# Kernel optimization log

Measured on AMD Instinct MI355X. Metric: run time of the kernel, lower is better.

Reference implementation:

```python
import jax, jax.numpy as jnp
import numpy as np

WIDTH = 1024
HEAD = 64


def setup_inputs() -> dict:
    key = jax.random.key(0)
    ks = jax.random.split(key, 8)
    B, S = 8, 2048
    x = jax.random.normal(ks[0], (B, S, WIDTH), dtype=jnp.float32)
    attn_mask = jnp.ones((B, S), dtype=jnp.int32)
    s = WIDTH ** -0.5
    Wq = jax.random.normal(ks[1], (WIDTH, HEAD), dtype=jnp.float32) * s
    bq = jnp.zeros((HEAD,), dtype=jnp.float32)
    Wk = jax.random.normal(ks[2], (WIDTH, HEAD), dtype=jnp.float32) * s
    bk = jnp.zeros((HEAD,), dtype=jnp.float32)
    Wv = jax.random.normal(ks[3], (WIDTH, HEAD), dtype=jnp.float32) * s
    bv = jnp.zeros((HEAD,), dtype=jnp.float32)
    return {"x": x, "attn_mask": attn_mask, "Wq": Wq, "bq": bq,
            "Wk": Wk, "bk": bk, "Wv": Wv, "bv": bv}


def reference(x, attn_mask, Wq, bq, Wk, bk, Wv, bv):
    # x: [B, S, width]; attn_mask: [B, S] (key padding mask)
    scale = HEAD ** -0.5
    Q = x @ Wq + bq  # [B, S, H]
    K = x @ Wk + bk
    V = x @ Wv + bv
    scores = jnp.einsum('bqh,bkh->bqk', Q, K) * scale  # [B, S, S]
    mask = (attn_mask[:, None, :] != 0)  # [B, 1, S] broadcast over queries
    scores = jnp.where(mask, scores, -jnp.inf)
    A = jax.nn.softmax(scores, axis=-1)
    return jnp.einsum('bqk,bkh->bqh', A, V)
```

## Files before the change

### kernel.cpp

```cpp
#include <hip/hip_runtime.h>
#include <hip/hip_bf16.h>

#define BATCH 8
#define SEQ   2048
#define DMODEL 1024
#define HD    64

typedef __attribute__((ext_vector_type(8))) short bf16x8;
typedef __attribute__((ext_vector_type(4))) float f32x4;
typedef __attribute__((ext_vector_type(4))) int int4v;
typedef __attribute__((ext_vector_type(2))) unsigned uint2v;
typedef unsigned int u32;

__device__ inline unsigned short f2bf(float f) {
    unsigned u = __builtin_bit_cast(unsigned, f);
    unsigned r = (u + 0x7FFFu + ((u >> 16) & 1u)) >> 16;
    return (unsigned short)r;
}

__device__ inline unsigned cvtpk(float lo, float hi) {
    unsigned r;
    asm("v_cvt_pk_bf16_f32 %0, %1, %2" : "=v"(r) : "v"(lo), "v"(hi));
    return r;
}

__device__ inline void gl_lds16(const void* g, void* l) {
    __builtin_amdgcn_global_load_lds(
        (const __attribute__((address_space(1))) u32*)g,
        (__attribute__((address_space(3))) u32*)l, 16, 0, 0);
}

__global__ void prep_w(const float* __restrict__ Wq, const float* __restrict__ Wk,
                       const float* __restrict__ Wv, unsigned short* __restrict__ WFrag) {
    __shared__ float tt[64][65];
    int p = blockIdx.x >> 4;
    int t = blockIdx.x & 15;
    int k0 = t * 64;
    const float* W = (p == 0) ? Wq : (p == 1) ? Wk : Wv;
    int tid = threadIdx.x;
#pragma unroll
    for (int j = 0; j < 16; j++) {
        int idx = tid + j * 256;
        int r = idx >> 6, c = idx & 63;
        tt[r][c] = W[(size_t)(k0 + r) * HD + c];
    }
    __syncthreads();
#pragma unroll
    for (int gi = 0; gi < 2; gi++) {
        int g = tid * 2 + gi;
        int ln = g & 15, lg = (g >> 4) & 3, s = (g >> 6) & 1, n = (g >> 7) & 3;
        union { bf16x8 v; unsigned short u[8]; } pk;
#pragma unroll
        for (int e = 0; e < 8; e++)
            pk.u[e] = f2bf(tt[s * 32 + lg * 8 + e][n * 16 + ln]);
        *(bf16x8*)(WFrag + (((size_t)(p * 4 + n) * 16 + t) * 1024 + s * 512 + lg * 128 + ln * 8)) = pk.v;
    }
}

__global__ __launch_bounds__(256) void proj_kernel(
    const float* __restrict__ x,
    const float* __restrict__ bq, const float* __restrict__ bk, const float* __restrict__ bv,
    const unsigned short* __restrict__ WFrag,
    unsigned short* __restrict__ Q, unsigned short* __restrict__ K,
    unsigned short* __restrict__ VT) {

    __shared__ __align__(16) unsigned short Xls[2][32 * 64];

    int tid = threadIdx.x;
    int w = tid >> 6, lane = tid & 63;
    int lg = lane >> 4, ln = lane & 15;
    int m0 = blockIdx.x * 32;

    const unsigned short* wbase[3];
#pragma unroll
    for (int j = 0; j < 3; j++)
        wbase[j] = WFrag + (size_t)(w * 3 + j) * 16384 + lane * 8;

    f32x4 acc[2][3];
#pragma unroll
    for (int m = 0; m < 2; m++)
#pragma unroll
        for (int j = 0; j < 3; j++) acc[m][j] = (f32x4){0.f, 0.f, 0.f, 0.f};

    f32x4 xq[2][2];
    bf16x8 bset[2][6];

    auto loadX = [&](int set, int k0) {
#pragma unroll
        for (int i = 0; i < 2; i++) {
            int c = tid + i * 256;
            xq[set][i] = *(const f32x4*)(x + (size_t)(m0 + (c >> 4)) * DMODEL + k0 + (c & 15) * 4);
        }
    };
    auto writeX = [&](unsigned short* buf, int set) {
#pragma unroll
        for (int i = 0; i < 2; i++) {
            int c = tid + i * 256;
            int row = c >> 4, slot = (c & 15) >> 1, half = c & 1;
            uint2v pk;
            pk[0] = cvtpk(xq[set][i][0], xq[set][i][1]);
            pk[1] = cvtpk(xq[set][i][2], xq[set][i][3]);
            *(uint2v*)((char*)buf + row * 128 + ((slot ^ (row & 7)) << 4) + half * 8) = pk;
        }
    };
    auto loadB = [&](int set, int k0) {
        int tb = (k0 >> 6) * 1024;
#pragma unroll
        for (int s = 0; s < 2; s++)
#pragma unroll
            for (int j = 0; j < 3; j++)
                bset[set][s * 3 + j] = *(const bf16x8*)(wbase[j] + tb + s * 512);
    };

    loadX(0, 0);
    writeX(&Xls[0][0], 0);
    loadX(1, 64);
    loadX(0, 128);
    loadB(0, 0);
    loadB(1, 64);
    __syncthreads();

#pragma unroll
    for (int t = 0; t < 16; t++) {
        const int cur = t & 1;
        const char* xb = (const char*)&Xls[cur][0];

#pragma unroll
        for (int s = 0; s < 2; s++) {
            bf16x8 a[2];
#pragma unroll
            for (int m = 0; m < 2; m++) {
                int row = m * 16 + ln;
                a[m] = *(const bf16x8*)(xb + row * 128 + (((s * 4 + lg) ^ (row & 7)) << 4));
            }
            __builtin_amdgcn_s_setprio(1);
#pragma unroll
            for (int m = 0; m < 2; m++)
#pragma unroll
                for (int j = 0; j < 3; j++)
                    acc[m][j] = __builtin_amdgcn_mfma_f32_16x16x32_bf16(a[m], bset[cur][s * 3 + j], acc[m][j], 0, 0, 0);
            __builtin_amdgcn_s_setprio(0);
        }

        if (t + 2 < 16) loadB(cur, (t + 2) * 64);
        if (t < 15) {
            writeX(&Xls[cur ^ 1][0], (t + 1) & 1);
            if (t + 3 < 16) loadX((t + 1) & 1, (t + 3) * 64);
        }
        __syncthreads();
    }

#pragma unroll
    for (int j = 0; j < 3; j++) {
        int f = w * 3 + j;
        int p = f >> 2, n = f & 3;
        int col = n * 16 + ln;
        const float* bias = (p == 0) ? bq : (p == 1) ? bk : bv;
        float bb = bias[col];
#pragma unroll
        for (int m = 0; m < 2; m++) {
#pragma unroll
            for (int r = 0; r < 4; r++) {
                float v = acc[m][j][r] + bb;
                int grow = m0 + m * 16 + lg * 4 + r;
                if (p == 0)      Q[(size_t)grow * HD + col] = f2bf(v);
                else if (p == 1) K[(size_t)grow * HD + col] = f2bf(v);
                else {
                    int b2 = grow >> 11, srow = grow & (SEQ - 1);
                    VT[((size_t)b2 * HD + col) * SEQ + srow] = f2bf(v);
                }
            }
        }
    }
}

__device__ inline void stage_tile(int tid, const unsigned short* Kb, const unsigned short* VTb,
                                  int kt, unsigned short* kbuf, unsigned short* vbuf) {
#pragma unroll
    for (int i = 0; i < 2; i++) {
        int d = tid * 16 + i * 4096;
        int row = d >> 7, slot = (d >> 4) & 7;
        const unsigned short* src = Kb + (size_t)(kt + row) * HD + ((slot ^ (row & 7)) << 3);
        gl_lds16(src, (char*)kbuf + d);
    }
#pragma unroll
    for (int i = 0; i < 2; i++) {
        int d = tid * 16 + i * 4096;
        int row = d >> 7, slot = (d >> 4) & 7;
        const unsigned short* src = VTb + (size_t)row * SEQ + kt + ((slot ^ (row & 7)) << 3);
        gl_lds16(src, (char*)vbuf + d);
    }
}

__global__ __launch_bounds__(256, 4) void attn_kernel(
    const unsigned short* __restrict__ Q, const unsigned short* __restrict__ K,
    const unsigned short* __restrict__ VT, const int* __restrict__ mask,
    float* __restrict__ out,
    unsigned short* __restrict__ Op, float* __restrict__ Mp, float* __restrict__ Lp,
    int nsplit) {

    __shared__ __align__(16) unsigned short Kls[2][64 * 64];
    __shared__ __align__(16) unsigned short Vls[2][64 * 64];
    __shared__ __align__(16) unsigned short plds_[4][16 * 64];

    int tid = threadIdx.x;
    int w = tid >> 6, lane = tid & 63;
    int lg = lane >> 4, ln = lane & 15;
    int b = blockIdx.y;
    int kh = blockIdx.z;
    int q0 = blockIdx.x * 64 + w * 16;
    int ntiles = 32 / nsplit;
    int kt0 = kh * ntiles * 64;

    const float SC = 0.125f * 1.44269504088896f;

    const int* mb = mask + b * SEQ;

    bf16x8 qf[2];
    {
        const unsigned short* qptr = Q + ((size_t)b * SEQ + q0 + ln) * HD + lg * 8;
        qf[0] = *(const bf16x8*)(qptr);
        qf[1] = *(const bf16x8*)(qptr + 32);
    }

    f32x4 o[4];
#pragma unroll
    for (int n = 0; n < 4; n++) o[n] = (f32x4){0.f, 0.f, 0.f, 0.f};
    float mrun = -1e38f, lrun = 0.f;

    const unsigned short* Kb = K + (size_t)b * SEQ * HD;
    const unsigned short* VTb = VT + (size_t)b * HD * SEQ;

    unsigned short* kcur = &Kls[0][0]; unsigned short* knx = &Kls[1][0];
    unsigned short* vcur = &Vls[0][0]; unsigned short* vnx = &Vls[1][0];
    char* pl = (char*)&plds_[w][0];
    const int swz = (ln & 7) << 4;

    stage_tile(tid, Kb, VTb, kt0, kcur, vcur);
    __syncthreads();

#pragma unroll 2
    for (int tt = 0; tt < ntiles; ++tt) {
        int kt = kt0 + tt * 64;
        if (tt < ntiles - 1) stage_tile(tid, Kb, VTb, kt + 64, knx, vnx);

        int4v mi[4];
#pragma unroll
        for (int n = 0; n < 4; ++n)
            mi[n] = *(const int4v*)(mb + kt + n * 16 + lg * 4);

        f32x4 st[4];
        const char* kb = (const char*)kcur;
        __builtin_amdgcn_s_setprio(1);
#pragma unroll
        for (int n = 0; n < 4; ++n) {
            int rb = (n * 16 + ln) * 128;
            bf16x8 ka0 = *(const bf16x8*)(kb + ((rb + lg * 16) ^ swz));
            bf16x8 ka1 = *(const bf16x8*)(kb + ((rb + 64 + lg * 16) ^ swz));
            f32x4 z = (f32x4){0.f, 0.f, 0.f, 0.f};
            st[n] = __builtin_amdgcn_mfma_f32_16x16x32_bf16(ka0, qf[0], z, 0, 0, 0);
            st[n] = __builtin_amdgcn_mfma_f32_16x16x32_bf16(ka1, qf[1], st[n], 0, 0, 0);
        }
        __builtin_amdgcn_s_setprio(0);

#pragma unroll
        for (int n = 0; n < 4; ++n)
#pragma unroll
            for (int r = 0; r < 4; ++r)
                st[n][r] = fmaf(st[n][r], SC, mi[n][r] ? 0.f : -1e30f);

        f32x4 mx = st[0];
#pragma unroll
        for (int n = 1; n < 4; ++n)
#pragma unroll
            for (int r = 0; r < 4; ++r) mx[r] = fmaxf(mx[r], st[n][r]);
        float pmax = fmaxf(fmaxf(mx[0], mx[1]), fmaxf(mx[2], mx[3]));
        pmax = fmaxf(pmax, __shfl_xor(pmax, 16));
        pmax = fmaxf(pmax, __shfl_xor(pmax, 32));

        if (!__all(pmax <= mrun + 8.f)) {
            float mnew = fmaxf(mrun, pmax);
            float corr = exp2f(mrun - mnew);
            mrun = mnew;
            lrun *= corr;
            float c0 = __shfl(corr, lg * 4 + 0);
            float c1 = __shfl(corr, lg * 4 + 1);
            float c2 = __shfl(corr, lg * 4 + 2);
            float c3 = __shfl(corr, lg * 4 + 3);
#pragma unroll
            for (int n = 0; n < 4; ++n) {
                o[n][0] *= c0; o[n][1] *= c1; o[n][2] *= c2; o[n][3] *= c3;
            }
        }

        f32x4 sv = (f32x4){0.f, 0.f, 0.f, 0.f};
#pragma unroll
        for (int n = 0; n < 4; ++n)
#pragma unroll
            for (int r = 0; r < 4; ++r) {
                float pp = exp2f(st[n][r] - mrun);
                st[n][r] = pp;
                sv[r] += pp;
            }
        float ts = (sv[0] + sv[1]) + (sv[2] + sv[3]);
        ts += __shfl_xor(ts, 16);
        ts += __shfl_xor(ts, 32);
        lrun += ts;

#pragma unroll
        for (int n = 0; n < 4; ++n) {
            uint2v ww;
            ww[0] = cvtpk(st[n][0], st[n][1]);
            ww[1] = cvtpk(st[n][2], st[n][3]);
            *(uint2v*)(pl + ((ln * 128 + n * 32 + lg * 8) ^ swz)) = ww;
        }
        asm volatile("s_waitcnt lgkmcnt(0)" ::: "memory");
        __builtin_amdgcn_sched_barrier(0);
        bf16x8 pa0 = *(const bf16x8*)(pl + ((ln * 128 + lg * 16) ^ swz));
        bf16x8 pa1 = *(const bf16x8*)(pl + ((ln * 128 + 64 + lg * 16) ^ swz));

        const char* vb = (const char*)vcur;
        __builtin_amdgcn_s_setprio(1);
#pragma unroll
        for (int n = 0; n < 4; ++n) {
            int rb = (n * 16 + ln) * 128;
            bf16x8 v0 = *(const bf16x8*)(vb + ((rb + lg * 16) ^ swz));
            bf16x8 v1 = *(const bf16x8*)(vb + ((rb + 64 + lg * 16) ^ swz));
            o[n] = __builtin_amdgcn_mfma_f32_16x16x32_bf16(pa0, v0, o[n], 0, 0, 0);
            o[n] = __builtin_amdgcn_mfma_f32_16x16x32_bf16(pa1, v1, o[n], 0, 0, 0);
        }
        __builtin_amdgcn_s_setprio(0);

        __syncthreads();
        unsigned short* tk = kcur; kcur = knx; knx = tk;
        unsigned short* tv = vcur; vcur = vnx; vnx = tv;
    }

    if (nsplit == 1) {
#pragma unroll
        for (int r = 0; r < 4; r++) {
            float Lr = __shfl(lrun, lg * 4 + r);
            float inv = 1.0f / Lr;
            int row = q0 + lg * 4 + r;
#pragma unroll
            for (int n = 0; n < 4; n++)
                out[((size_t)b * SEQ + row) * HD + n * 16 + ln] = o[n][r] * inv;
        }
    } else {
        size_t base = (size_t)kh * BATCH * SEQ * HD;
#pragma unroll
        for (int r = 0; r < 4; r++) {
            int row = q0 + lg * 4 + r;
            size_t gr = (size_t)b * SEQ + row;
#pragma unroll
            for (int n = 0; n < 4; n++)
                Op[base + gr * HD + n * 16 + ln] = f2bf(o[n][r]);
        }
        if (lane < 16) {
            size_t gr = (size_t)b * SEQ + q0 + ln;
            Mp[(size_t)kh * BATCH * SEQ + gr] = mrun;
            Lp[(size_t)kh * BATCH * SEQ + gr] = lrun;
        }
    }
}

__global__ __launch_bounds__(256) void combine_kernel(
    const unsigned short* __restrict__ Op, const float* __restrict__ Mp,
    const float* __restrict__ Lp, float* __restrict__ out) {
    int g = blockIdx.x * 256 + threadIdx.x;
    int row = g >> 3;
    int c0 = (g & 7) * 8;
    const int NR = BATCH * SEQ;

    float m[4], l[4];
#pragma unroll
    for (int s = 0; s < 4; s++) {
        m[s] = Mp[(size_t)s * NR + row];
        l[s] = Lp[(size_t)s * NR + row];
    }
    float M = fmaxf(fmaxf(m[0], m[1]), fmaxf(m[2], m[3]));
    float e[4], L = 0.f;
#pragma unroll
    for (int s = 0; s < 4; s++) { e[s] = exp2f(m[s] - M); L += l[s] * e[s]; }
    float inv = 1.0f / L;

    float acc[8] = {0.f, 0.f, 0.f, 0.f, 0.f, 0.f, 0.f, 0.f};
#pragma unroll
    for (int s = 0; s < 4; s++) {
        bf16x8 ov = *(const bf16x8*)(Op + ((size_t)s * NR + row) * HD + c0);
#pragma unroll
        for (int i = 0; i < 8; i++) {
            float f = __builtin_bit_cast(float, ((u32)(unsigned short)ov[i]) << 16);
            acc[i] += f * e[s];
        }
    }
    f32x4 r0, r1;
#pragma unroll
    for (int i = 0; i < 4; i++) { r0[i] = acc[i] * inv; r1[i] = acc[4 + i] * inv; }
    *(f32x4*)(out + (size_t)row * HD + c0) = r0;
    *(f32x4*)(out + (size_t)row * HD + c0 + 4) = r1;
}

extern "C" void kernel_launch(void* const* d_in, const int* in_sizes, int n_in,
                              void* d_out, int out_size, void* d_ws, size_t ws_size,
                              hipStream_t stream) {
    const float* x  = (const float*)d_in[0];
    const int*   am = (const int*)d_in[1];
    const float* Wq = (const float*)d_in[2];
    const float* bq = (const float*)d_in[3];
    const float* Wk = (const float*)d_in[4];
    const float* bk = (const float*)d_in[5];
    const float* Wv = (const float*)d_in[6];
    const float* bv = (const float*)d_in[7];
    float* out = (float*)d_out;

    unsigned short* ws = (unsigned short*)d_ws;
    unsigned short* Wt  = ws;
    unsigned short* Qw  = ws + 3 * HD * DMODEL;
    unsigned short* Kw  = Qw + (size_t)BATCH * SEQ * HD;
    unsigned short* VTw = Kw + (size_t)BATCH * SEQ * HD;
    size_t base_sh = 3 * HD * DMODEL + 3 * (size_t)BATCH * SEQ * HD;
    unsigned short* Op = ws + base_sh;
    float* Mp = (float*)(Op + 4 * (size_t)BATCH * SEQ * HD);
    float* Lp = Mp + 4 * (size_t)BATCH * SEQ;
    size_t need = base_sh * 2 + 4 * (size_t)BATCH * SEQ * HD * 2
                + 8 * (size_t)BATCH * SEQ * 4;

    int nsplit = (ws_size >= need) ? 4 : 1;

    prep_w<<<48, 256, 0, stream>>>(Wq, Wk, Wv, Wt);
    proj_kernel<<<(BATCH * SEQ) / 32, 256, 0, stream>>>(x, bq, bk, bv, Wt, Qw, Kw, VTw);
    attn_kernel<<<dim3(SEQ / 64, BATCH, nsplit), 256, 0, stream>>>(Qw, Kw, VTw, am, out,
                                                                   Op, Mp, Lp, nsplit);
    if (nsplit == 4)
        combine_kernel<<<(BATCH * SEQ * 8) / 256, 256, 0, stream>>>(Op, Mp, Lp, out);
}
```

Measured before the change: 55.63 us.

## Load x directly into MFMA A-fragments in projection kernel, drop LDS staging

The projection kernel no longer stages x through shared memory with barriers. Each lane now reads its fp32 A-fragment rows straight from global memory, converts them to bf16 in registers and feeds the MFMAs, using a two-set register ping-pong for prefetch. Launch bounds are set to 2 blocks per CU. This removes the LDS writes and reads and the per-step __syncthreads, but each lane's global loads are less coalesced (16 rows per wave, 32 bytes per lane per chunk) and more registers are held live.

```diff
diff --git a/kernel.cpp b/kernel.cpp
--- a/kernel.cpp
+++ b/kernel.cpp
@@ -57,15 +57,13 @@
     }
 }
 
-__global__ __launch_bounds__(256) void proj_kernel(
+__global__ __launch_bounds__(256, 2) void proj_kernel(
     const float* __restrict__ x,
     const float* __restrict__ bq, const float* __restrict__ bk, const float* __restrict__ bv,
     const unsigned short* __restrict__ WFrag,
     unsigned short* __restrict__ Q, unsigned short* __restrict__ K,
     unsigned short* __restrict__ VT) {
 
-    __shared__ __align__(16) unsigned short Xls[2][32 * 64];
-
     int tid = threadIdx.x;
     int w = tid >> 6, lane = tid & 63;
     int lg = lane >> 4, ln = lane & 15;
@@ -76,78 +74,64 @@
     for (int j = 0; j < 3; j++)
         wbase[j] = WFrag + (size_t)(w * 3 + j) * 16384 + lane * 8;
 
+    const float* xr0 = x + (size_t)(m0 + ln) * DMODEL + lg * 8;
+    const float* xr1 = x + (size_t)(m0 + 16 + ln) * DMODEL + lg * 8;
+
     f32x4 acc[2][3];
 #pragma unroll
     for (int m = 0; m < 2; m++)
 #pragma unroll
         for (int j = 0; j < 3; j++) acc[m][j] = (f32x4){0.f, 0.f, 0.f, 0.f};
 
-    f32x4 xq[2][2];
-    bf16x8 bset[2][6];
-
-    auto loadX = [&](int set, int k0) {
-#pragma unroll
-        for (int i = 0; i < 2; i++) {
-            int c = tid + i * 256;
-            xq[set][i] = *(const f32x4*)(x + (size_t)(m0 + (c >> 4)) * DMODEL + k0 + (c & 15) * 4);
-        }
+    bf16x8 bA[6], bB[6];
+    f32x4 xA[8], xB[8];
+
+    auto LB = [&](bf16x8* d, int t) {
+#pragma unroll
+        for (int s = 0; s < 2; s++)
+#pragma unroll
+            for (int j = 0; j < 3; j++)
+                d[s * 3 + j] = *(const bf16x8*)(wbase[j] + t * 1024 + s * 512);
     };
-    auto writeX = [&](unsigned short* buf, int set) {
-#pragma unroll
-        for (int i = 0; i < 2; i++) {
-            int c = tid + i * 256;
-            int row = c >> 4, slot = (c & 15) >> 1, half = c & 1;
-            uint2v pk;
-            pk[0] = cvtpk(xq[set][i][0], xq[set][i][1]);
-            pk[1] = cvtpk(xq[set][i][2], xq[set][i][3]);
-            *(uint2v*)((char*)buf + row * 128 + ((slot ^ (row & 7)) << 4) + half * 8) = pk;
-        }
+    auto LX = [&](f32x4* d, int t) {
+        int k0 = t * 64;
+        d[0] = *(const f32x4*)(xr0 + k0);      d[1] = *(const f32x4*)(xr0 + k0 + 4);
+        d[2] = *(const f32x4*)(xr1 + k0);      d[3] = *(const f32x4*)(xr1 + k0 + 4);
+        d[4] = *(const f32x4*)(xr0 + k0 + 32); d[5] = *(const f32x4*)(xr0 + k0 + 36);
+        d[6] = *(const f32x4*)(xr1 + k0 + 32); d[7] = *(const f32x4*)(xr1 + k0 + 36);
     };
-    auto loadB = [&](int set, int k0) {
-        int tb = (k0 >> 6) * 1024;
-#pragma unroll
-        for (int s = 0; s < 2; s++)
-#pragma unroll
-            for (int j = 0; j < 3; j++)
-                bset[set][s * 3 + j] = *(const bf16x8*)(wbase[j] + tb + s * 512);
+    auto CP = [&](const f32x4* xd, const bf16x8* bd) {
+#pragma unroll
+        for (int s = 0; s < 2; s++) {
+            union { bf16x8 v; unsigned u[4]; } a0, a1;
+            a0.u[0] = cvtpk(xd[s * 4 + 0][0], xd[s * 4 + 0][1]);
+            a0.u[1] = cvtpk(xd[s * 4 + 0][2], xd[s * 4 + 0][3]);
+            a0.u[2] = cvtpk(xd[s * 4 + 1][0], xd[s * 4 + 1][1]);
+            a0.u[3] = cvtpk(xd[s * 4 + 1][2], xd[s * 4 + 1][3]);
+            a1.u[0] = cvtpk(xd[s * 4 + 2][0], xd[s * 4 + 2][1]);
+            a1.u[1] = cvtpk(xd[s * 4 + 2][2], xd[s * 4 + 2][3]);
+            a1.u[2] = cvtpk(xd[s * 4 + 3][0], xd[s * 4 + 3][1]);
+            a1.u[3] = cvtpk(xd[s * 4 + 3][2], xd[s * 4 + 3][3]);
+#pragma unroll
+            for (int j = 0; j < 3; j++) {
+                acc[0][j] = __builtin_amdgcn_mfma_f32_16x16x32_bf16(a0.v, bd[s * 3 + j], acc[0][j], 0, 0, 0);
+                acc[1][j] = __builtin_amdgcn_mfma_f32_16x16x32_bf16(a1.v, bd[s * 3 + j], acc[1][j], 0, 0, 0);
+            }
+        }
     };
 
-    loadX(0, 0);
-    writeX(&Xls[0][0], 0);
-    loadX(1, 64);
-    loadX(0, 128);
-    loadB(0, 0);
-    loadB(1, 64);
-    __syncthreads();
-
-#pragma unroll
-    for (int t = 0; t < 16; t++) {
-        const int cur = t & 1;
-        const char* xb = (const char*)&Xls[cur][0];
-
-#pragma unroll
-        for (int s = 0; s < 2; s++) {
-            bf16x8 a[2];
-#pragma unroll
-            for (int m = 0; m < 2; m++) {
-                int row = m * 16 + ln;
-                a[m] = *(const bf16x8*)(xb + row * 128 + (((s * 4 + lg) ^ (row & 7)) << 4));
-            }
-            __builtin_amdgcn_s_setprio(1);
-#pragma unroll
-            for (int m = 0; m < 2; m++)
-#pragma unroll
-                for (int j = 0; j < 3; j++)
-                    acc[m][j] = __builtin_amdgcn_mfma_f32_16x16x32_bf16(a[m], bset[cur][s * 3 + j], acc[m][j], 0, 0, 0);
-            __builtin_amdgcn_s_setprio(0);
-        }
-
-        if (t + 2 < 16) loadB(cur, (t + 2) * 64);
-        if (t < 15) {
-            writeX(&Xls[cur ^ 1][0], (t + 1) & 1);
-            if (t + 3 < 16) loadX((t + 1) & 1, (t + 3) * 64);
-        }
-        __syncthreads();
+    LX(xA, 0);
+    LB(bA, 0);
+#pragma unroll 1
+    for (int t = 0; t < 16; t += 2) {
+        LX(xB, t + 1);
+        LB(bB, t + 1);
+        CP(xA, bA);
+        if (t + 2 < 16) {
+            LX(xA, t + 2);
+            LB(bA, t + 2);
+        }
+        CP(xB, bB);
     }
 
 #pragma unroll
```

Result: slower. 76.70 us (+37.9%).

## Restructure projection K-loop into 128-wide tiles with ping-pong register sets

Applied to the files above, without the earlier changes.

The projection kernel now stages 128-column x tiles in LDS, using a 16-way XOR swizzle instead of 64-column tiles. It replaces the fully unrolled 16-step loop with a rolled 4-iteration loop that alternates two explicit register sets for x and B fragments. It also adds a launch_bounds minimum of 2 blocks per SM and drops the s_setprio hints. The goal is fewer barriers per K element and more overlap of global loads with MFMA work, at the cost of more registers per thread, which the occupancy hint may force to spill.

```diff
diff --git a/kernel.cpp b/kernel.cpp
--- a/kernel.cpp
+++ b/kernel.cpp
@@ -57,14 +57,14 @@
     }
 }
 
-__global__ __launch_bounds__(256) void proj_kernel(
+__global__ __launch_bounds__(256, 2) void proj_kernel(
     const float* __restrict__ x,
     const float* __restrict__ bq, const float* __restrict__ bk, const float* __restrict__ bv,
     const unsigned short* __restrict__ WFrag,
     unsigned short* __restrict__ Q, unsigned short* __restrict__ K,
     unsigned short* __restrict__ VT) {
 
-    __shared__ __align__(16) unsigned short Xls[2][32 * 64];
+    __shared__ __align__(16) unsigned short Xls[2][32 * 128];
 
     int tid = threadIdx.x;
     int w = tid >> 6, lane = tid & 63;
@@ -82,71 +82,71 @@
 #pragma unroll
         for (int j = 0; j < 3; j++) acc[m][j] = (f32x4){0.f, 0.f, 0.f, 0.f};
 
-    f32x4 xq[2][2];
-    bf16x8 bset[2][6];
-
-    auto loadX = [&](int set, int k0) {
-#pragma unroll
-        for (int i = 0; i < 2; i++) {
+    f32x4 xA[4], xB[4];
+    bf16x8 bA[12], bB[12];
+
+    auto loadX = [&](f32x4* xr, int tile) {
+#pragma unroll
+        for (int i = 0; i < 4; i++) {
             int c = tid + i * 256;
-            xq[set][i] = *(const f32x4*)(x + (size_t)(m0 + (c >> 4)) * DMODEL + k0 + (c & 15) * 4);
+            xr[i] = *(const f32x4*)(x + (size_t)(m0 + (c >> 5)) * DMODEL + tile * 128 + (c & 31) * 4);
         }
     };
-    auto writeX = [&](unsigned short* buf, int set) {
-#pragma unroll
-        for (int i = 0; i < 2; i++) {
+    auto writeX = [&](unsigned short* buf, const f32x4* xr) {
+#pragma unroll
+        for (int i = 0; i < 4; i++) {
             int c = tid + i * 256;
-            int row = c >> 4, slot = (c & 15) >> 1, half = c & 1;
+            int row = c >> 5, cc = c & 31;
             uint2v pk;
-            pk[0] = cvtpk(xq[set][i][0], xq[set][i][1]);
-            pk[1] = cvtpk(xq[set][i][2], xq[set][i][3]);
-            *(uint2v*)((char*)buf + row * 128 + ((slot ^ (row & 7)) << 4) + half * 8) = pk;
+            pk[0] = cvtpk(xr[i][0], xr[i][1]);
+            pk[1] = cvtpk(xr[i][2], xr[i][3]);
+            *(uint2v*)((char*)buf + row * 256 + (((cc >> 1) ^ (row & 15)) << 4) + (c & 1) * 8) = pk;
         }
     };
-    auto loadB = [&](int set, int k0) {
-        int tb = (k0 >> 6) * 1024;
-#pragma unroll
-        for (int s = 0; s < 2; s++)
+    auto loadB = [&](bf16x8* d, int ph) {
+#pragma unroll
+        for (int s = 0; s < 4; s++)
 #pragma unroll
             for (int j = 0; j < 3; j++)
-                bset[set][s * 3 + j] = *(const bf16x8*)(wbase[j] + tb + s * 512);
+                d[s * 3 + j] = *(const bf16x8*)(wbase[j] + (2 * ph + (s >> 1)) * 1024 + (s & 1) * 512);
     };
-
-    loadX(0, 0);
-    writeX(&Xls[0][0], 0);
-    loadX(1, 64);
-    loadX(0, 128);
-    loadB(0, 0);
-    loadB(1, 64);
-    __syncthreads();
-
-#pragma unroll
-    for (int t = 0; t < 16; t++) {
-        const int cur = t & 1;
-        const char* xb = (const char*)&Xls[cur][0];
-
-#pragma unroll
-        for (int s = 0; s < 2; s++) {
+    auto COMPUTE = [&](const unsigned short* buf, const bf16x8* bd) {
+        const char* xb = (const char*)buf;
+#pragma unroll
+        for (int s = 0; s < 4; s++) {
             bf16x8 a[2];
 #pragma unroll
             for (int m = 0; m < 2; m++) {
                 int row = m * 16 + ln;
-                a[m] = *(const bf16x8*)(xb + row * 128 + (((s * 4 + lg) ^ (row & 7)) << 4));
+                a[m] = *(const bf16x8*)(xb + row * 256 + ((((s << 2) + lg) ^ (row & 15)) << 4));
             }
-            __builtin_amdgcn_s_setprio(1);
-#pragma unroll
-            for (int m = 0; m < 2; m++)
-#pragma unroll
-                for (int j = 0; j < 3; j++)
-                    acc[m][j] = __builtin_amdgcn_mfma_f32_16x16x32_bf16(a[m], bset[cur][s * 3 + j], acc[m][j], 0, 0, 0);
-            __builtin_amdgcn_s_setprio(0);
-        }
-
-        if (t + 2 < 16) loadB(cur, (t + 2) * 64);
-        if (t < 15) {
-            writeX(&Xls[cur ^ 1][0], (t + 1) & 1);
-            if (t + 3 < 16) loadX((t + 1) & 1, (t + 3) * 64);
-        }
+#pragma unroll
+            for (int j = 0; j < 3; j++) {
+                acc[0][j] = __builtin_amdgcn_mfma_f32_16x16x32_bf16(a[0], bd[s * 3 + j], acc[0][j], 0, 0, 0);
+                acc[1][j] = __builtin_amdgcn_mfma_f32_16x16x32_bf16(a[1], bd[s * 3 + j], acc[1][j], 0, 0, 0);
+            }
+        }
+    };
+
+    loadX(xA, 0);
+    loadB(bA, 0);
+    writeX(&Xls[0][0], xA);
+    loadX(xB, 1);
+    __syncthreads();
+
+#pragma unroll 1
+    for (int p = 0; p < 4; p++) {
+        writeX(&Xls[1][0], xB);
+        if (p < 3) loadX(xA, 2 * p + 2);
+        loadB(bB, 2 * p + 1);
+        COMPUTE(&Xls[0][0], bA);
+        __syncthreads();
+        if (p < 3) {
+            writeX(&Xls[0][0], xA);
+            loadX(xB, 2 * p + 3);
+            loadB(bA, 2 * p + 2);
+        }
+        COMPUTE(&Xls[1][0], bB);
         __syncthreads();
     }
 
```

Result: no change. 56.19 us (+1.0%).
